# Kernel optimization log

Measured on AMD Instinct MI355X. Metric: run time of the kernel, lower is better.

## Reference

```python
import jax, jax.numpy as jnp
import numpy as np

H = 64
V = 50257
B = 32
L = 4096
LN_EPS = 1e-5
DELTA_EPS = 1e-6


def setup_inputs() -> dict:
    key = jax.random.key(0)
    ks = jax.random.split(key, 10)
    s = 0.02
    return {
        "seq": jax.random.randint(ks[0], (B, L), 0, V),
        "read_pos": -1,
        "embed": jax.random.normal(ks[1], (V, H), jnp.float32) * s,
        "w1": jax.random.normal(ks[2], (H, 2 * H), jnp.float32) * s,
        "b1": jnp.zeros((2 * H,), jnp.float32),
        "w2": jax.random.normal(ks[3], (2 * H, H), jnp.float32) * s,
        "b2": jnp.zeros((H,), jnp.float32),
        "ln_g": jnp.ones((H,), jnp.float32),
        "ln_b": jnp.zeros((H,), jnp.float32),
        "rp_w": jax.random.normal(ks[4], (H, H), jnp.float32) * s,
        "rp_b": jnp.zeros((H,), jnp.float32),
        "out_w": jax.random.normal(ks[5], (H, V), jnp.float32) * s,
        "out_b": jnp.zeros((V,), jnp.float32),
    }


def _encoder(seq, embed, w1, b1, w2, b2, ln_g, ln_b):
    e = embed[seq]  # [B, L, H]
    f = jnp.maximum(e @ w1 + b1, 0.0) @ w2 + b2  # FFN
    x = e + f
    mu = jnp.mean(x, axis=-1, keepdims=True)
    var = jnp.mean((x - mu) ** 2, axis=-1, keepdims=True)
    return (x - mu) * jax.lax.rsqrt(var + LN_EPS) * ln_g + ln_b


def _delta_memory(h_all):
    # Strictly sequential delta-rule fast-weight update over t = 0..L-2.
    Bs, Ls, Hs = h_all.shape
    keys = jnp.transpose(h_all[:, : Ls - 1, :], (1, 0, 2))  # [L-1, B, H]

    def step(M, k):
        vp = jnp.einsum('bij,bj->bi', M, k)  # M @ k
        u = k - vp / (jnp.sum(k * k, axis=-1, keepdims=True) + DELTA_EPS)
        M = M + u[:, :, None] * k[:, None, :]  # outer product update
        return M, None

    M0 = jnp.zeros((Bs, Hs, Hs), h_all.dtype)
    M, _ = jax.lax.scan(step, M0, keys)
    return M


def reference(seq, read_pos, embed, w1, b1, w2, b2, ln_g, ln_b, rp_w, rp_b, out_w, out_b):
    h_all = _encoder(seq, embed, w1, b1, w2, b2, ln_g, ln_b)  # [B, L, H]
    M = _delta_memory(h_all)  # [B, H, H]
    q = h_all[:, read_pos, :]  # [B, H]
    r = jnp.einsum('bij,bj->bi', M, q)
    return (r @ rp_w + rp_b) @ out_w + out_b  # [B, V]
```

## Files before the change

### kernel.cpp

```cpp
#include <hip/hip_runtime.h>

#define HH 64
#define VV 50257
#define BB 32
#define LL 4096

constexpr float LN_EPS_F = 1e-5f;
constexpr float DELTA_EPS_F = 1e-6f;

constexpr int CS = 64;
constexpr int NG = LL / CS;

typedef float f32x4 __attribute__((ext_vector_type(4)));
typedef short bf16x8 __attribute__((ext_vector_type(8)));
union U16x8 { uint4 u; bf16x8 v; unsigned short s[8]; };

__device__ __forceinline__ unsigned short f2bf(float f) {
  union { float f; unsigned u; } v; v.f = f;
  unsigned r = v.u + 0x7fff + ((v.u >> 16) & 1);
  return (unsigned short)(r >> 16);
}

template <int CTRL>
__device__ __forceinline__ float dpp_add(float x) {
  int t = __builtin_amdgcn_update_dpp(0, __float_as_int(x), CTRL, 0xF, 0xF, true);
  return x + __int_as_float(t);
}

__device__ __forceinline__ float wave_sum_lane63(float x) {
  x = dpp_add<0x111>(x);
  x = dpp_add<0x112>(x);
  x = dpp_add<0x114>(x);
  x = dpp_add<0x118>(x);
  x = dpp_add<0x142>(x);
  x = dpp_add<0x143>(x);
  return x;
}

__device__ __forceinline__ float readlane_f(float x, int lane) {
  return __int_as_float(__builtin_amdgcn_readlane(__float_as_int(x), lane));
}

__global__ __launch_bounds__(256) void prep_kernel(
    const float* __restrict__ w1, const float* __restrict__ w2,
    unsigned short* __restrict__ w1b, unsigned short* __restrict__ w2b) {
  int i = blockIdx.x * 256 + threadIdx.x;
  if (i < 8192) {
    int jj = i >> 6, h = i & 63;
    w1b[i] = f2bf(w1[h * 128 + jj]);
  } else {
    int k = i - 8192;
    int h = k >> 7, jj = k & 127;
    w2b[k] = f2bf(w2[jj * 64 + h]);
  }
}

__global__ __launch_bounds__(64, 1) void encoder_kernel(
    const int* __restrict__ seq, const float* __restrict__ embed,
    const unsigned short* __restrict__ w1b, const float* __restrict__ b1,
    const unsigned short* __restrict__ w2b, const float* __restrict__ b2,
    const float* __restrict__ ln_g, const float* __restrict__ ln_b,
    float* __restrict__ h_all, float* __restrict__ beta) {
  __shared__ __align__(16) char pool[26624];
  unsigned short (*e_l)[72] = reinterpret_cast<unsigned short (*)[72]>(pool);
  unsigned short (*act_l)[136] = reinterpret_cast<unsigned short (*)[136]>(pool + 9216);
  float (*x_l)[65] = reinterpret_cast<float (*)[65]>(pool);
  __shared__ float2 gb_l[64];
  __shared__ float b1_l[128], b2_l[64];

  int lane = threadIdx.x;
  int q = lane >> 4, l = lane & 15;
  int base = blockIdx.x * 64;
  int s = seq[base + lane];

  {
    const float4* ep = reinterpret_cast<const float4*>(embed + (size_t)s * HH);
#pragma unroll
    for (int i = 0; i < 8; ++i) {
      float4 va = ep[2 * i], vb = ep[2 * i + 1];
      uint4 u;
      u.x = (unsigned)f2bf(va.x) | ((unsigned)f2bf(va.y) << 16);
      u.y = (unsigned)f2bf(va.z) | ((unsigned)f2bf(va.w) << 16);
      u.z = (unsigned)f2bf(vb.x) | ((unsigned)f2bf(vb.y) << 16);
      u.w = (unsigned)f2bf(vb.z) | ((unsigned)f2bf(vb.w) << 16);
      *(uint4*)&e_l[lane][8 * i] = u;
    }
  }
  gb_l[lane] = make_float2(ln_g[lane], ln_b[lane]);
  b1_l[lane] = b1[lane];
  b1_l[64 + lane] = b1[64 + lane];
  b2_l[lane] = b2[lane];

  bf16x8 af1[8][2];
#pragma unroll
  for (int mi = 0; mi < 8; ++mi)
#pragma unroll
    for (int ks = 0; ks < 2; ++ks) {
      U16x8 t;
      t.u = *(const uint4*)(w1b + (mi * 16 + l) * 64 + ks * 32 + q * 8);
      af1[mi][ks] = t.v;
    }

  __syncthreads();

  f32x4 acc1[8][4];
#pragma unroll
  for (int mi = 0; mi < 8; ++mi)
#pragma unroll
    for (int nt = 0; nt < 4; ++nt) acc1[mi][nt] = (f32x4){0.f, 0.f, 0.f, 0.f};

#pragma unroll
  for (int ks = 0; ks < 2; ++ks) {
    bf16x8 bfr[4];
#pragma unroll
    for (int nt = 0; nt < 4; ++nt) {
      U16x8 t;
      t.u = *(const uint4*)&e_l[nt * 16 + l][ks * 32 + q * 8];
      bfr[nt] = t.v;
    }
#pragma unroll
    for (int mi = 0; mi < 8; ++mi)
#pragma unroll
      for (int nt = 0; nt < 4; ++nt)
        acc1[mi][nt] = __builtin_amdgcn_mfma_f32_16x16x32_bf16(
            af1[mi][ks], bfr[nt], acc1[mi][nt], 0, 0, 0);
  }

#pragma unroll
  for (int mi = 0; mi < 8; ++mi)
#pragma unroll
    for (int nt = 0; nt < 4; ++nt) {
      int tok = nt * 16 + l;
      int jj0 = mi * 16 + q * 4;
      float v0 = fmaxf(acc1[mi][nt][0] + b1_l[jj0 + 0], 0.f);
      float v1 = fmaxf(acc1[mi][nt][1] + b1_l[jj0 + 1], 0.f);
      float v2 = fmaxf(acc1[mi][nt][2] + b1_l[jj0 + 2], 0.f);
      float v3 = fmaxf(acc1[mi][nt][3] + b1_l[jj0 + 3], 0.f);
      uint2 u;
      u.x = (unsigned)f2bf(v0) | ((unsigned)f2bf(v1) << 16);
      u.y = (unsigned)f2bf(v2) | ((unsigned)f2bf(v3) << 16);
      *(uint2*)&act_l[tok][jj0] = u;
    }

  bf16x8 bf2[4][4];
#pragma unroll
  for (int nt = 0; nt < 4; ++nt)
#pragma unroll
    for (int ks = 0; ks < 4; ++ks) {
      U16x8 t;
      t.u = *(const uint4*)(w2b + (nt * 16 + l) * 128 + ks * 32 + q * 8);
      bf2[nt][ks] = t.v;
    }

  __syncthreads();

  f32x4 acc2[4][4];
#pragma unroll
  for (int mt = 0; mt < 4; ++mt)
#pragma unroll
    for (int nt = 0; nt < 4; ++nt) acc2[mt][nt] = (f32x4){0.f, 0.f, 0.f, 0.f};

#pragma unroll
  for (int ks = 0; ks < 4; ++ks) {
    bf16x8 afr[4];
#pragma unroll
    for (int mt = 0; mt < 4; ++mt) {
      U16x8 t;
      t.u = *(const uint4*)&act_l[mt * 16 + l][ks * 32 + q * 8];
      afr[mt] = t.v;
    }
#pragma unroll
    for (int mt = 0; mt < 4; ++mt)
#pragma unroll
      for (int nt = 0; nt < 4; ++nt)
        acc2[mt][nt] = __builtin_amdgcn_mfma_f32_16x16x32_bf16(
            afr[mt], bf2[nt][ks], acc2[mt][nt], 0, 0, 0);
  }

  __syncthreads();

#pragma unroll
  for (int mt = 0; mt < 4; ++mt)
#pragma unroll
    for (int nt = 0; nt < 4; ++nt) {
      int h = nt * 16 + l;
#pragma unroll
      for (int r = 0; r < 4; ++r) {
        int tok = mt * 16 + q * 4 + r;
        x_l[tok][h] = acc2[mt][nt][r] + b2_l[h];
      }
    }

  __syncthreads();

  float x[HH];
#pragma unroll
  for (int h = 0; h < HH; ++h) x[h] = x_l[lane][h];
  {
    const float4* ep = reinterpret_cast<const float4*>(embed + (size_t)s * HH);
#pragma unroll
    for (int i = 0; i < 16; ++i) {
      float4 v = ep[i];
      x[4 * i + 0] += v.x; x[4 * i + 1] += v.y;
      x[4 * i + 2] += v.z; x[4 * i + 3] += v.w;
    }
  }
  float sum = 0.f;
#pragma unroll
  for (int h = 0; h < HH; ++h) sum += x[h];
  float mu = sum * (1.f / HH);
  float vs = 0.f;
#pragma unroll
  for (int h = 0; h < HH; ++h) { float dx = x[h] - mu; vs = fmaf(dx, dx, vs); }
  float rstd = rsqrtf(vs * (1.f / HH) + LN_EPS_F);

  float ss = 0.f;
#pragma unroll
  for (int h = 0; h < HH; ++h) {
    float2 gb = gb_l[h];
    float o = fmaf((x[h] - mu) * rstd, gb.x, gb.y);
    ss = fmaf(o, o, ss);
    x[h] = o;
  }
  float4* hp = reinterpret_cast<float4*>(h_all + (size_t)(base + lane) * HH);
#pragma unroll
  for (int i = 0; i < 16; ++i)
    hp[i] = make_float4(x[4 * i + 0], x[4 * i + 1], x[4 * i + 2], x[4 * i + 3]);
  beta[base + lane] = 1.f / (ss + DELTA_EPS_F);
}

__global__ __launch_bounds__(64, 1) void gram_n_kernel(
    const float* __restrict__ h_all, const float* __restrict__ beta,
    float* __restrict__ Ng) {
  __shared__ __align__(16) char smem[37120];
  unsigned short (*pA)[64][72] = reinterpret_cast<unsigned short (*)[64][72]>(smem);
  unsigned short (*pB)[64][72] = reinterpret_cast<unsigned short (*)[64][72]>(smem + 18432);
  float (*Gl)[68] = reinterpret_cast<float (*)[68]>(smem + 18432);
  float* bl = reinterpret_cast<float*>(smem + 36864);

  int c = blockIdx.x, b = blockIdx.y, lane = threadIdx.x;
  int q = lane >> 4, l = lane & 15;
  const float* src = h_all + ((size_t)b * LL + c * CS) * HH;

#pragma unroll
  for (int i = 0; i < 16; ++i) {
    int row = i * 4 + q;
    float4 v = *(const float4*)&src[row * 64 + l * 4];
    float f[4] = {v.x, v.y, v.z, v.w};
    unsigned hs[4], ls[4];
#pragma unroll
    for (int r = 0; r < 4; ++r) {
      unsigned short hb = f2bf(f[r]);
      float hf = __uint_as_float(((unsigned)hb) << 16);
      hs[r] = hb; ls[r] = f2bf(f[r] - hf);
    }
    *(uint2*)&pA[0][row][l * 4] = make_uint2(hs[0] | (hs[1] << 16), hs[2] | (hs[3] << 16));
    *(uint2*)&pA[1][row][l * 4] = make_uint2(ls[0] | (ls[1] << 16), ls[2] | (ls[3] << 16));
  }
  bl[lane] = beta[(size_t)b * LL + c * CS + lane];
  if (c == NG - 1) { pA[0][63][lane] = 0; pA[1][63][lane] = 0; }
  __syncthreads();

  f32x4 acc[4][4];
#pragma unroll
  for (int mi = 0; mi < 4; ++mi)
#pragma unroll
    for (int nt = 0; nt < 4; ++nt) acc[mi][nt] = (f32x4){0.f, 0.f, 0.f, 0.f};

#pragma unroll
  for (int ks = 0; ks < 2; ++ks) {
    bf16x8 ah[4], al_[4];
#pragma unroll
    for (int i = 0; i < 4; ++i) {
      U16x8 t;
      t.u = *(const uint4*)&pA[0][i * 16 + l][ks * 32 + q * 8]; ah[i] = t.v;
      t.u = *(const uint4*)&pA[1][i * 16 + l][ks * 32 + q * 8]; al_[i] = t.v;
    }
#pragma unroll
    for (int mi = 0; mi < 4; ++mi)
#pragma unroll
      for (int nt = 0; nt < 4; ++nt) {
        acc[mi][nt] = __builtin_amdgcn_mfma_f32_16x16x32_bf16(ah[mi], ah[nt], acc[mi][nt], 0, 0, 0);
        acc[mi][nt] = __builtin_amdgcn_mfma_f32_16x16x32_bf16(ah[mi], al_[nt], acc[mi][nt], 0, 0, 0);
        acc[mi][nt] = __builtin_amdgcn_mfma_f32_16x16x32_bf16(al_[mi], ah[nt], acc[mi][nt], 0, 0, 0);
      }
  }

#pragma unroll
  for (int mi = 0; mi < 4; ++mi) {
    int s0 = mi * 16 + q * 4;
    float4 b4 = *(const float4*)&bl[s0];
#pragma unroll
    for (int nt = 0; nt < 4; ++nt) {
      int t = nt * 16 + l;
      Gl[s0 + 0][t] = acc[mi][nt][0] * b4.x;
      Gl[s0 + 1][t] = acc[mi][nt][1] * b4.y;
      Gl[s0 + 2][t] = acc[mi][nt][2] * b4.z;
      Gl[s0 + 3][t] = acc[mi][nt][3] * b4.w;
    }
  }
  __syncthreads();

  float m[64];
#pragma unroll
  for (int t = 0; t < 64; ++t) m[t] = src[t * 64 + lane];
  if (c == NG - 1) m[63] = 0.f;

#pragma unroll
  for (int i = 0; i < 32; ++i) {
    float v0 = m[2 * i], v1 = m[2 * i + 1];
    unsigned short h0 = f2bf(v0), h1 = f2bf(v1);
    float r0 = v0 - __uint_as_float(((unsigned)h0) << 16);
    float r1 = v1 - __uint_as_float(((unsigned)h1) << 16);
    *(unsigned*)&pA[0][lane][2 * i] = (unsigned)h0 | (((unsigned)h1) << 16);
    *(unsigned*)&pA[1][lane][2 * i] = (unsigned)f2bf(r0) | (((unsigned)f2bf(r1)) << 16);
  }

#pragma unroll
  for (int s = 63; s >= 1; --s) {
    float ms = m[s];
    const float* g = &Gl[s][0];
#pragma unroll
    for (int i = 0; i + 3 < s; i += 4) {
      float4 g4 = *(const float4*)(g + i);
      m[i + 0] = fmaf(-g4.x, ms, m[i + 0]);
      m[i + 1] = fmaf(-g4.y, ms, m[i + 1]);
      m[i + 2] = fmaf(-g4.z, ms, m[i + 2]);
      m[i + 3] = fmaf(-g4.w, ms, m[i + 3]);
    }
    for (int t = s & ~3; t < s; ++t) m[t] = fmaf(-g[t], ms, m[t]);
  }

  __syncthreads();

#pragma unroll
  for (int i = 0; i < 32; ++i) {
    float v0 = bl[2 * i] * m[2 * i];
    float v1 = bl[2 * i + 1] * m[2 * i + 1];
    unsigned short h0 = f2bf(v0), h1 = f2bf(v1);
    float r0 = v0 - __uint_as_float(((unsigned)h0) << 16);
    float r1 = v1 - __uint_as_float(((unsigned)h1) << 16);
    *(unsigned*)&pB[0][lane][2 * i] = (unsigned)h0 | (((unsigned)h1) << 16);
    *(unsigned*)&pB[1][lane][2 * i] = (unsigned)f2bf(r0) | (((unsigned)f2bf(r1)) << 16);
  }
  __syncthreads();

  f32x4 acc2[4][4];
#pragma unroll
  for (int mi = 0; mi < 4; ++mi)
#pragma unroll
    for (int nt = 0; nt < 4; ++nt) acc2[mi][nt] = (f32x4){0.f, 0.f, 0.f, 0.f};

#pragma unroll
  for (int ks = 0; ks < 2; ++ks) {
    bf16x8 ah[4], al_[4], bh[4], blo[4];
#pragma unroll
    for (int i = 0; i < 4; ++i) {
      U16x8 t;
      t.u = *(const uint4*)&pA[0][i * 16 + l][ks * 32 + q * 8]; ah[i] = t.v;
      t.u = *(const uint4*)&pA[1][i * 16 + l][ks * 32 + q * 8]; al_[i] = t.v;
      t.u = *(const uint4*)&pB[0][i * 16 + l][ks * 32 + q * 8]; bh[i] = t.v;
      t.u = *(const uint4*)&pB[1][i * 16 + l][ks * 32 + q * 8]; blo[i] = t.v;
    }
#pragma unroll
    for (int mi = 0; mi < 4; ++mi)
#pragma unroll
      for (int nt = 0; nt < 4; ++nt) {
        acc2[mi][nt] = __builtin_amdgcn_mfma_f32_16x16x32_bf16(ah[mi], bh[nt], acc2[mi][nt], 0, 0, 0);
        acc2[mi][nt] = __builtin_amdgcn_mfma_f32_16x16x32_bf16(ah[mi], blo[nt], acc2[mi][nt], 0, 0, 0);
        acc2[mi][nt] = __builtin_amdgcn_mfma_f32_16x16x32_bf16(al_[mi], bh[nt], acc2[mi][nt], 0, 0, 0);
      }
  }

  float* np = Ng + (((size_t)b * NG + c) << 12);
#pragma unroll
  for (int mi = 0; mi < 4; ++mi)
#pragma unroll
    for (int nt = 0; nt < 4; ++nt) {
      int h0 = mi * 16 + q * 4, hp = nt * 16 + l;
      float4 v;
      v.x = ((h0 + 0 == hp) ? 1.f : 0.f) - acc2[mi][nt][0];
      v.y = ((h0 + 1 == hp) ? 1.f : 0.f) - acc2[mi][nt][1];
      v.z = ((h0 + 2 == hp) ? 1.f : 0.f) - acc2[mi][nt][2];
      v.w = ((h0 + 3 == hp) ? 1.f : 0.f) - acc2[mi][nt][3];
      *(float4*)&np[hp * 64 + h0] = v;
    }
}

__global__ __launch_bounds__(64, 1) void boundary_kernel(
    const float* __restrict__ h_all, const float* __restrict__ Ng,
    const int* __restrict__ read_pos_p, float* __restrict__ Qg) {
  __shared__ __align__(16) float nt0[64 * 64];
  __shared__ __align__(16) float nt1[64 * 64];
  __shared__ __align__(16) float ql[64];

  int b = blockIdx.x, lane = threadIdx.x;
  int rpv = read_pos_p[0];
  int pos = rpv < 0 ? rpv + LL : rpv;
  float Q = h_all[((size_t)b * LL + pos) * HH + lane];

  const float* Nb = Ng + ((size_t)b * NG << 12);

  auto load_chunk = [&](float* buf, int c) {
    const float* g = Nb + ((size_t)c << 12);
#pragma unroll
    for (int i = 0; i < 16; ++i)
      __builtin_amdgcn_global_load_lds(
          (const __attribute__((address_space(1))) unsigned*)(g + i * 256 + lane * 4),
          (__attribute__((address_space(3))) unsigned*)(buf + i * 256), 16, 0, 0);
  };

  auto step = [&](const float* buf, int c, bool last) {
    if (last) __builtin_amdgcn_s_waitcnt(0x0F70);
    else      __builtin_amdgcn_s_waitcnt(0x4F70);
    Qg[((size_t)b * NG + c) * HH + lane] = Q;
    ql[lane] = Q;
    float a0 = 0.f, a1 = 0.f, a2 = 0.f, a3 = 0.f;
#pragma unroll
    for (int j = 0; j < 64; j += 4) {
      float4 q4 = *(const float4*)&ql[j];
      a0 = fmaf(buf[(j + 0) * 64 + lane], q4.x, a0);
      a1 = fmaf(buf[(j + 1) * 64 + lane], q4.y, a1);
      a2 = fmaf(buf[(j + 2) * 64 + lane], q4.z, a2);
      a3 = fmaf(buf[(j + 3) * 64 + lane], q4.w, a3);
    }
    Q = (a0 + a1) + (a2 + a3);
  };

  load_chunk(nt1, NG - 1);
  load_chunk(nt0, NG - 2);

#pragma unroll 1
  for (int c = NG - 1; c >= 1; c -= 2) {
    step(nt1, c, false);
    __builtin_amdgcn_s_waitcnt(0xC07F);
    if (c >= 3) load_chunk(nt1, c - 2);
    step(nt0, c - 1, c == 1);
    __builtin_amdgcn_s_waitcnt(0xC07F);
    if (c >= 3) load_chunk(nt0, c - 3);
  }
}

__global__ __launch_bounds__(64, 1) void chunk_scan_kernel(
    const float* __restrict__ h_all, const float* __restrict__ beta,
    const float* __restrict__ Qg, float* __restrict__ rc) {
  int c = blockIdx.x, b = blockIdx.y, j = threadIdx.x;
  const float* hb = h_all + (size_t)b * LL * HH;
  const float* betab = beta + (size_t)b * LL;

  float P = Qg[((size_t)b * NG + c) * HH + j];
  float r = 0.f;

  float kk[CS];
#pragma unroll
  for (int i = 0; i < CS; ++i) kk[i] = hb[((size_t)(c * CS + i)) * HH + j];
  float bv = betab[c * CS + j];

  bool last = (c == NG - 1);
#pragma unroll
  for (int i = CS - 1; i >= 0; --i) {
    float k = kk[i];
    float bt = readlane_f(bv, i);
    float m = k * P;
    float s = wave_sum_lane63(m);
    float d = readlane_f(s, 63);
    if (i == CS - 1 && last) d = 0.f;
    r = fmaf(d, k, r);
    P = fmaf(-(bt * d), k, P);
  }
  rc[((size_t)b * NG + c) * HH + j] = r;
}

__global__ __launch_bounds__(64, 1) void combine_kernel(
    const float* __restrict__ rc, const float* __restrict__ rp_w,
    const float* __restrict__ rp_b, float* __restrict__ yv) {
  int b = blockIdx.x, j = threadIdx.x;
  float r = 0.f;
#pragma unroll 8
  for (int cc = 0; cc < NG; ++cc) r += rc[((size_t)b * NG + cc) * HH + j];
  __shared__ float rs[HH];
  rs[j] = r;
  __syncthreads();
  float yj = rp_b[j];
#pragma unroll
  for (int h = 0; h < HH; ++h) yj = fmaf(rs[h], rp_w[h * HH + j], yj);
  yv[b * HH + j] = yj;
}

__global__ __launch_bounds__(256, 2) void out_kernel(
    const float* __restrict__ yv, const float* __restrict__ out_w,
    const float* __restrict__ out_b, float* __restrict__ out) {
  __shared__ float ys[BB * HH];
  for (int i = threadIdx.x; i < BB * HH; i += 256) ys[i] = yv[i];
  __syncthreads();

  int v = blockIdx.x * 256 + threadIdx.x;
  if (v >= VV) return;

  float acc[BB];
  float ob = out_b[v];
#pragma unroll
  for (int b = 0; b < BB; ++b) acc[b] = ob;

  for (int h = 0; h < HH; ++h) {
    float w = out_w[(size_t)h * VV + v];
#pragma unroll
    for (int b = 0; b < BB; ++b) acc[b] = fmaf(ys[b * HH + h], w, acc[b]);
  }
#pragma unroll
  for (int b = 0; b < BB; ++b) out[(size_t)b * VV + v] = acc[b];
}

extern "C" void kernel_launch(void* const* d_in, const int* in_sizes, int n_in,
                              void* d_out, int out_size, void* d_ws, size_t ws_size,
                              hipStream_t stream) {
  (void)in_sizes; (void)n_in; (void)out_size; (void)ws_size;
  const int*   seq   = (const int*)d_in[0];
  const int*   rp    = (const int*)d_in[1];
  const float* embed = (const float*)d_in[2];
  const float* w1    = (const float*)d_in[3];
  const float* b1    = (const float*)d_in[4];
  const float* w2    = (const float*)d_in[5];
  const float* b2    = (const float*)d_in[6];
  const float* ln_g  = (const float*)d_in[7];
  const float* ln_b  = (const float*)d_in[8];
  const float* rp_w  = (const float*)d_in[9];
  const float* rp_b  = (const float*)d_in[10];
  const float* out_w = (const float*)d_in[11];
  const float* out_b = (const float*)d_in[12];
  float* out = (float*)d_out;

  float* h_all = (float*)d_ws;
  float* beta  = h_all + (size_t)BB * LL * HH;
  float* Ng    = beta + (size_t)BB * LL;
  float* Qg    = Ng + (size_t)BB * NG * HH * HH;
  float* rcv   = Qg + (size_t)BB * NG * HH;
  float* yv    = rcv + (size_t)BB * NG * HH;
  unsigned short* w1b = (unsigned short*)(yv + (size_t)BB * HH);
  unsigned short* w2b = w1b + 8192;

  prep_kernel<<<64, 256, 0, stream>>>(w1, w2, w1b, w2b);
  encoder_kernel<<<BB * LL / 64, 64, 0, stream>>>(seq, embed, w1b, b1, w2b, b2,
                                                  ln_g, ln_b, h_all, beta);
  gram_n_kernel<<<dim3(NG, BB), 64, 0, stream>>>(h_all, beta, Ng);
  boundary_kernel<<<BB, 64, 0, stream>>>(h_all, Ng, rp, Qg);
  chunk_scan_kernel<<<dim3(NG, BB), 64, 0, stream>>>(h_all, beta, Qg, rcv);
  combine_kernel<<<BB, 64, 0, stream>>>(rcv, rp_w, rp_b, yv);
  out_kernel<<<(VV + 255) / 256, 256, 0, stream>>>(yv, out_w, out_b, out);
}
```

Measured before the change: 229.7 us.

## Cut encoder LDS and registers, use bf16 Gram tile, interleave N layout

The encoder's shared pool shrinks by aliasing the activation buffer onto the embedding buffer, and weight fragments are loaded just in time instead of held in registers. Launch bounds now allow two blocks per CU. The Gram kernel stores the scaled Gram tile in bf16 to halve LDS traffic in the triangular solve, which loses precision in that solve. The N matrices are written in an interleaved layout so the boundary kernel can read float4 vectors from LDS instead of scalar loads.

```diff
diff --git a/kernel.cpp b/kernel.cpp
--- a/kernel.cpp
+++ b/kernel.cpp
@@ -55,15 +55,15 @@
   }
 }
 
-__global__ __launch_bounds__(64, 1) void encoder_kernel(
+__global__ __launch_bounds__(64, 2) void encoder_kernel(
     const int* __restrict__ seq, const float* __restrict__ embed,
     const unsigned short* __restrict__ w1b, const float* __restrict__ b1,
     const unsigned short* __restrict__ w2b, const float* __restrict__ b2,
     const float* __restrict__ ln_g, const float* __restrict__ ln_b,
     float* __restrict__ h_all, float* __restrict__ beta) {
-  __shared__ __align__(16) char pool[26624];
+  __shared__ __align__(16) char pool[17408];
   unsigned short (*e_l)[72] = reinterpret_cast<unsigned short (*)[72]>(pool);
-  unsigned short (*act_l)[136] = reinterpret_cast<unsigned short (*)[136]>(pool + 9216);
+  unsigned short (*act_l)[136] = reinterpret_cast<unsigned short (*)[136]>(pool);
   float (*x_l)[65] = reinterpret_cast<float (*)[65]>(pool);
   __shared__ float2 gb_l[64];
   __shared__ float b1_l[128], b2_l[64];
@@ -90,41 +90,36 @@
   b1_l[lane] = b1[lane];
   b1_l[64 + lane] = b1[64 + lane];
   b2_l[lane] = b2[lane];
-
-  bf16x8 af1[8][2];
-#pragma unroll
-  for (int mi = 0; mi < 8; ++mi)
-#pragma unroll
-    for (int ks = 0; ks < 2; ++ks) {
-      U16x8 t;
-      t.u = *(const uint4*)(w1b + (mi * 16 + l) * 64 + ks * 32 + q * 8);
-      af1[mi][ks] = t.v;
-    }
-
-  __syncthreads();
-
-  f32x4 acc1[8][4];
-#pragma unroll
-  for (int mi = 0; mi < 8; ++mi)
-#pragma unroll
-    for (int nt = 0; nt < 4; ++nt) acc1[mi][nt] = (f32x4){0.f, 0.f, 0.f, 0.f};
-
-#pragma unroll
-  for (int ks = 0; ks < 2; ++ks) {
-    bf16x8 bfr[4];
+  __syncthreads();
+
+  bf16x8 bfr[2][4];
+#pragma unroll
+  for (int ks = 0; ks < 2; ++ks)
 #pragma unroll
     for (int nt = 0; nt < 4; ++nt) {
       U16x8 t;
       t.u = *(const uint4*)&e_l[nt * 16 + l][ks * 32 + q * 8];
-      bfr[nt] = t.v;
-    }
-#pragma unroll
-    for (int mi = 0; mi < 8; ++mi)
+      bfr[ks][nt] = t.v;
+    }
+  __syncthreads();
+
+  f32x4 acc1[8][4];
+#pragma unroll
+  for (int mi = 0; mi < 8; ++mi)
+#pragma unroll
+    for (int nt = 0; nt < 4; ++nt) acc1[mi][nt] = (f32x4){0.f, 0.f, 0.f, 0.f};
+
+#pragma unroll
+  for (int ks = 0; ks < 2; ++ks)
+#pragma unroll
+    for (int mi = 0; mi < 8; ++mi) {
+      U16x8 t;
+      t.u = *(const uint4*)(w1b + (mi * 16 + l) * 64 + ks * 32 + q * 8);
 #pragma unroll
       for (int nt = 0; nt < 4; ++nt)
         acc1[mi][nt] = __builtin_amdgcn_mfma_f32_16x16x32_bf16(
-            af1[mi][ks], bfr[nt], acc1[mi][nt], 0, 0, 0);
-  }
+            t.v, bfr[ks][nt], acc1[mi][nt], 0, 0, 0);
+    }
 
 #pragma unroll
   for (int mi = 0; mi < 8; ++mi)
@@ -141,17 +136,6 @@
       u.y = (unsigned)f2bf(v2) | ((unsigned)f2bf(v3) << 16);
       *(uint2*)&act_l[tok][jj0] = u;
     }
-
-  bf16x8 bf2[4][4];
-#pragma unroll
-  for (int nt = 0; nt < 4; ++nt)
-#pragma unroll
-    for (int ks = 0; ks < 4; ++ks) {
-      U16x8 t;
-      t.u = *(const uint4*)(w2b + (nt * 16 + l) * 128 + ks * 32 + q * 8);
-      bf2[nt][ks] = t.v;
-    }
-
   __syncthreads();
 
   f32x4 acc2[4][4];
@@ -170,13 +154,15 @@
       afr[mt] = t.v;
     }
 #pragma unroll
-    for (int mt = 0; mt < 4; ++mt)
-#pragma unroll
-      for (int nt = 0; nt < 4; ++nt)
+    for (int nt = 0; nt < 4; ++nt) {
+      U16x8 t2;
+      t2.u = *(const uint4*)(w2b + (nt * 16 + l) * 128 + ks * 32 + q * 8);
+#pragma unroll
+      for (int mt = 0; mt < 4; ++mt)
         acc2[mt][nt] = __builtin_amdgcn_mfma_f32_16x16x32_bf16(
-            afr[mt], bf2[nt][ks], acc2[mt][nt], 0, 0, 0);
-  }
-
+            afr[mt], t2.v, acc2[mt][nt], 0, 0, 0);
+    }
+  }
   __syncthreads();
 
 #pragma unroll
@@ -190,7 +176,6 @@
         x_l[tok][h] = acc2[mt][nt][r] + b2_l[h];
       }
     }
-
   __syncthreads();
 
   float x[HH];
@@ -235,7 +220,7 @@
   __shared__ __align__(16) char smem[37120];
   unsigned short (*pA)[64][72] = reinterpret_cast<unsigned short (*)[64][72]>(smem);
   unsigned short (*pB)[64][72] = reinterpret_cast<unsigned short (*)[64][72]>(smem + 18432);
-  float (*Gl)[68] = reinterpret_cast<float (*)[68]>(smem + 18432);
+  unsigned short (*Glb)[72] = reinterpret_cast<unsigned short (*)[72]>(smem + 18432);
   float* bl = reinterpret_cast<float*>(smem + 36864);
 
   int c = blockIdx.x, b = blockIdx.y, lane = threadIdx.x;
@@ -293,10 +278,10 @@
 #pragma unroll
     for (int nt = 0; nt < 4; ++nt) {
       int t = nt * 16 + l;
-      Gl[s0 + 0][t] = acc[mi][nt][0] * b4.x;
-      Gl[s0 + 1][t] = acc[mi][nt][1] * b4.y;
-      Gl[s0 + 2][t] = acc[mi][nt][2] * b4.z;
-      Gl[s0 + 3][t] = acc[mi][nt][3] * b4.w;
+      Glb[s0 + 0][t] = f2bf(acc[mi][nt][0] * b4.x);
+      Glb[s0 + 1][t] = f2bf(acc[mi][nt][1] * b4.y);
+      Glb[s0 + 2][t] = f2bf(acc[mi][nt][2] * b4.z);
+      Glb[s0 + 3][t] = f2bf(acc[mi][nt][3] * b4.w);
     }
   }
   __syncthreads();
@@ -319,18 +304,21 @@
 #pragma unroll
   for (int s = 63; s >= 1; --s) {
     float ms = m[s];
-    const float* g = &Gl[s][0];
-#pragma unroll
-    for (int i = 0; i + 3 < s; i += 4) {
-      float4 g4 = *(const float4*)(g + i);
-      m[i + 0] = fmaf(-g4.x, ms, m[i + 0]);
-      m[i + 1] = fmaf(-g4.y, ms, m[i + 1]);
-      m[i + 2] = fmaf(-g4.z, ms, m[i + 2]);
-      m[i + 3] = fmaf(-g4.w, ms, m[i + 3]);
-    }
-    for (int t = s & ~3; t < s; ++t) m[t] = fmaf(-g[t], ms, m[t]);
-  }
-
+    const unsigned short* g = &Glb[s][0];
+#pragma unroll
+    for (int i = 0; i < 64; i += 8) {
+      if (i < s) {
+        uint4 u = *(const uint4*)(g + i);
+        unsigned w[4] = {u.x, u.y, u.z, u.w};
+#pragma unroll
+        for (int p = 0; p < 4; ++p) {
+          int t0 = i + 2 * p, t1 = t0 + 1;
+          if (t0 < s) m[t0] = fmaf(-__uint_as_float(w[p] << 16), ms, m[t0]);
+          if (t1 < s) m[t1] = fmaf(-__uint_as_float(w[p] & 0xFFFF0000u), ms, m[t1]);
+        }
+      }
+    }
+  }
   __syncthreads();
 
 #pragma unroll
@@ -377,13 +365,13 @@
   for (int mi = 0; mi < 4; ++mi)
 #pragma unroll
     for (int nt = 0; nt < 4; ++nt) {
-      int h0 = mi * 16 + q * 4, hp = nt * 16 + l;
-      float4 v;
-      v.x = ((h0 + 0 == hp) ? 1.f : 0.f) - acc2[mi][nt][0];
-      v.y = ((h0 + 1 == hp) ? 1.f : 0.f) - acc2[mi][nt][1];
-      v.z = ((h0 + 2 == hp) ? 1.f : 0.f) - acc2[mi][nt][2];
-      v.w = ((h0 + 3 == hp) ? 1.f : 0.f) - acc2[mi][nt][3];
-      *(float4*)&np[hp * 64 + h0] = v;
+      int h0 = mi * 16 + q * 4, j = nt * 16 + l;
+      int base2 = (j >> 2) * 256 + (j & 3);
+#pragma unroll
+      for (int r = 0; r < 4; ++r) {
+        int h = h0 + r;
+        np[base2 + h * 4] = ((h == j) ? 1.f : 0.f) - acc2[mi][nt][r];
+      }
     }
 }
 
@@ -417,12 +405,11 @@
     ql[lane] = Q;
     float a0 = 0.f, a1 = 0.f, a2 = 0.f, a3 = 0.f;
 #pragma unroll
-    for (int j = 0; j < 64; j += 4) {
-      float4 q4 = *(const float4*)&ql[j];
-      a0 = fmaf(buf[(j + 0) * 64 + lane], q4.x, a0);
-      a1 = fmaf(buf[(j + 1) * 64 + lane], q4.y, a1);
-      a2 = fmaf(buf[(j + 2) * 64 + lane], q4.z, a2);
-      a3 = fmaf(buf[(j + 3) * 64 + lane], q4.w, a3);
+    for (int j4 = 0; j4 < 16; ++j4) {
+      float4 q4 = *(const float4*)&ql[j4 * 4];
+      float4 nv = *(const float4*)&buf[j4 * 256 + lane * 4];
+      a0 = fmaf(nv.x, q4.x, a0); a1 = fmaf(nv.y, q4.y, a1);
+      a2 = fmaf(nv.z, q4.z, a2); a3 = fmaf(nv.w, q4.w, a3);
     }
     Q = (a0 + a1) + (a2 + a3);
   };
```

After: 338.4 us. +47.3%, slower.
